# Optimization experiments

Measured on AMD Instinct MI355X. Metric: run time of the kernel, lower is better.

The kernel has to match this reference:

```python
import jax, jax.numpy as jnp
import numpy as np

ALPHA = 0.2  # LeakyReLU negative slope used throughout
NEG = -9e15


def _leaky(x, a=ALPHA):
    return jnp.where(x >= 0, x, a * x)


def _gat_layer(h, adj, W, a, concat):
    # h: [N, Fin], W: [Fin, Fout], a: [2*Fout, 1]
    Wh = h @ W                                   # [N, Fout]
    d = W.shape[-1]
    e = _leaky(Wh @ a[:d] + (Wh @ a[d:]).T)      # [N, N]
    att = jax.nn.softmax(jnp.where(adj > 0, e, NEG), axis=1)
    out = att @ Wh                               # [N, Fout]
    return jax.nn.elu(out) if concat else out


def setup_inputs() -> dict:
    key = jax.random.key(0)
    ks = jax.random.split(key, 24)
    N, F, H, D1, O1 = 4096, 512, 4, 256, 64
    x = jax.random.normal(ks[0], (N, F), dtype=jnp.float32)
    adj = jax.random.bernoulli(ks[1], 0.02, (N, N))
    adj = (adj | adj.T | jnp.eye(N, dtype=bool)).astype(jnp.float32)
    observation = jax.random.randint(ks[2], (1, N), 0, 2, dtype=jnp.int32)
    s_mat = jax.random.uniform(ks[3], (N, N), dtype=jnp.float32)
    theta = jax.random.uniform(ks[4], (1, F), dtype=jnp.float32)
    g = lambda k, s, sc: (jax.random.normal(k, s, dtype=jnp.float32) * sc)
    return {
        'x': x, 'adj': adj, 'observation': observation, 's_mat': s_mat,
        'theta': theta,
        'Wh0': g(ks[5], (H, F, D1), 0.05), 'ah0': g(ks[6], (H, 2 * D1, 1), 0.05),
        'Wh1': g(ks[7], (H, D1, D1), 0.05), 'ah1': g(ks[8], (H, 2 * D1, 1), 0.05),
        'Wo0': g(ks[9], (H * D1, O1), 0.05), 'ao0': g(ks[10], (2 * O1, 1), 0.05),
        'Wo1': g(ks[11], (O1, 1), 0.2), 'ao1': g(ks[12], (2, 1), 0.2),
        'dW': g(ks[13], (2, 10), 0.5), 'dW0': g(ks[14], (1, 10), 0.5),
        'dW1': g(ks[15], (10, 20), 0.5), 'dW01': g(ks[16], (1, 20), 0.5),
        'dW2': g(ks[17], (20, 10), 0.5), 'dW02': g(ks[18], (1, 10), 0.5),
        'dV': g(ks[19], (10, 1), 0.5), 'dV0': g(ks[20], (1, 1), 0.5),
    }


def reference(x, adj, observation, s_mat, theta, Wh0, ah0, Wh1, ah1,
              Wo0, ao0, Wo1, ao1, dW, dW0, dW1, dW01, dW2, dW02, dV, dV0):
    # mergeState: add theta to rows in the seed set (observation[0] == 1)
    seed = (observation[0] == 1).astype(x.dtype)[:, None]  # [N,1]
    h_in = x + seed * theta

    # multi-head 2-layer attention stacks (concat=True -> elu inside)
    def head(W0, a0, W1, a1):
        h = _gat_layer(h_in, adj, W0, a0, True)
        return _gat_layer(h, adj, W1, a1, True)

    hh = jax.vmap(head)(Wh0, ah0, Wh1, ah1)                 # [H, N, D1]
    hcat = jnp.transpose(hh, (1, 0, 2)).reshape(h_in.shape[0], -1)  # [N, H*D1]

    # output attention stack (concat=False), then elu (GAT.forward)
    h = _gat_layer(hcat, adj, Wo0, ao0, False)
    h = _gat_layer(h, adj, Wo1, ao1, False)
    h_ = jax.nn.elu(h)                                      # [N, 1]

    # GAT_degree v2: degreeNN over [h_, degree]
    d_v = s_mat.sum(axis=1, keepdims=True)                  # [N, 1]
    x_ = jnp.concatenate([h_, d_v], axis=1)                 # [N, 2]
    h0 = _leaky(x_ @ dW + dW0)
    h1 = _leaky(h0 @ dW1 + dW01)
    h2 = _leaky(h1 @ dW2 + dW02)
    return _leaky(h2 @ dV + dV0)                            # [N, 1]
```

## Files before the change

kernel.cpp:

```cpp
#include <hip/hip_runtime.h>
#include <hip/hip_bf16.h>
#include <hip/hip_fp16.h>
#include <math.h>

#define MAXDEG 512

typedef short v8s __attribute__((ext_vector_type(8)));
typedef float v4f __attribute__((ext_vector_type(4)));
typedef _Float16 h2 __attribute__((ext_vector_type(2)));

__device__ __forceinline__ float blockReduceSum(float v) {
    __shared__ float sh[8];
    int lane = threadIdx.x & 63, w = threadIdx.x >> 6;
    for (int o = 32; o > 0; o >>= 1) v += __shfl_down(v, o);
    __syncthreads();
    if (lane == 0) sh[w] = v;
    __syncthreads();
    if (w == 0) {
        int nw = (blockDim.x + 63) >> 6;
        v = (lane < nw) ? sh[lane] : 0.f;
        for (int o = 4; o > 0; o >>= 1) v += __shfl_down(v, o);
        if (lane == 0) sh[0] = v;
    }
    __syncthreads();
    return sh[0];
}

__device__ __forceinline__ float blockReduceMax(float v) {
    __shared__ float sh[8];
    int lane = threadIdx.x & 63, w = threadIdx.x >> 6;
    for (int o = 32; o > 0; o >>= 1) v = fmaxf(v, __shfl_down(v, o));
    __syncthreads();
    if (lane == 0) sh[w] = v;
    __syncthreads();
    if (w == 0) {
        int nw = (blockDim.x + 63) >> 6;
        v = (lane < nw) ? sh[lane] : -3.4e38f;
        for (int o = 4; o > 0; o >>= 1) v = fmaxf(v, __shfl_down(v, o));
        if (lane == 0) sh[0] = v;
    }
    __syncthreads();
    return sh[0];
}


__global__ void csr_rowsum(const float* __restrict__ adj, const float* __restrict__ s,
                           int* __restrict__ colIdx, int* __restrict__ deg,
                           float* __restrict__ dv, int N) {
    int row = blockIdx.x;
    __shared__ int cnt;
    if (threadIdx.x == 0) cnt = 0;
    __syncthreads();
    const float4* ar = (const float4*)(adj + (size_t)row * N);
    const float4* sr = (const float4*)(s + (size_t)row * N);
    int* outp = colIdx + (size_t)row * MAXDEG;
    float psum = 0.f;
    const int n4 = N >> 2;
    for (int j4 = threadIdx.x; j4 < n4; j4 += blockDim.x) {
        float4 a4 = ar[j4];
        float4 s4 = sr[j4];
        psum += (s4.x + s4.y) + (s4.z + s4.w);
        int jb = j4 << 2;
        if (a4.x > 0.f) { int p = atomicAdd(&cnt, 1); if (p < MAXDEG) outp[p] = jb; }
        if (a4.y > 0.f) { int p = atomicAdd(&cnt, 1); if (p < MAXDEG) outp[p] = jb + 1; }
        if (a4.z > 0.f) { int p = atomicAdd(&cnt, 1); if (p < MAXDEG) outp[p] = jb + 2; }
        if (a4.w > 0.f) { int p = atomicAdd(&cnt, 1); if (p < MAXDEG) outp[p] = jb + 3; }
    }
    psum = blockReduceSum(psum);
    __syncthreads();
    if (threadIdx.x == 0) {
        deg[row] = cnt < MAXDEG ? cnt : MAXDEG;
        dv[row] = psum;
    }
}

__global__ void prep(const float* __restrict__ x, const int* __restrict__ obs,
                     const float* __restrict__ theta,
                     const float* __restrict__ Wh0, const float* __restrict__ Wh1,
                     const float* __restrict__ Wo0,
                     __half* __restrict__ hin, __half* __restrict__ Wh0t,
                     __half* __restrict__ Wh1t, __half* __restrict__ Wo0t,
                     float* __restrict__ elerZ, int elerN) {
    const int n0 = 4096 * 512;
    const int n1 = 4 * 512 * 256;
    const int n2 = 4 * 256 * 256;
    const int n3 = 1024 * 64;
    int i = blockIdx.x * 256 + threadIdx.x;
    if (i < n0) {
        int n = i >> 9, f = i & 511;
        float v = x[i];
        if (obs[n] == 1) v += theta[f];
        hin[i] = __float2half(v);
    } else if (i < n0 + n1) {
        int t = i - n0;
        int b = t / (512 * 256), r = t % (512 * 256);
        int mm = r >> 9, kk = r & 511;
        Wh0t[t] = __float2half(Wh0[b * 512 * 256 + kk * 256 + mm]);
    } else if (i < n0 + n1 + n2) {
        int t = i - n0 - n1;
        int b = t >> 16, r = t & 65535;
        int mm = r >> 8, kk = r & 255;
        Wh1t[t] = __float2half(Wh1[b * 65536 + kk * 256 + mm]);
    } else if (i < n0 + n1 + n2 + n3) {
        int t = i - n0 - n1 - n2;
        int mm = t >> 10, kk = t & 1023;
        Wo0t[t] = __float2half(Wo0[kk * 64 + mm]);
    } else if (i < n0 + n1 + n2 + n3 + elerN) {
        elerZ[i - n0 - n1 - n2 - n3] = 0.f;
    }
}

__global__ __launch_bounds__(256) void gemm_mfma128(
    const __half* __restrict__ A, const __half* __restrict__ Bt,
    __half* __restrict__ C, int N, int K, int M,
    size_t sA, size_t sB, size_t sC,
    const float* __restrict__ aVec, size_t aStride,
    float* __restrict__ el, float* __restrict__ er) {
    int b = blockIdx.z;
    const unsigned short* Ag = (const unsigned short*)(A + (size_t)b * sA);
    const unsigned short* Bg = (const unsigned short*)(Bt + (size_t)b * sB);
    __half* Cg = C + (size_t)b * sC;
    const float* av = aVec + (size_t)b * aStride;

    __shared__ __align__(16) unsigned short As[128][40];
    __shared__ __align__(16) unsigned short Bs[128][40];

    const int tid = threadIdx.x;
    const int wave = tid >> 6, lane = tid & 63;
    const int wm = wave >> 1, wn = wave & 1;
    const int row0 = blockIdx.y * 128, col0 = blockIdx.x * 128;
    const int lr = tid >> 2;
    const int lo = (tid & 3) * 8;
    const int m = lane & 15, quad = lane >> 4;

    v4f acc[4][4];
    #pragma unroll
    for (int i = 0; i < 4; i++)
        #pragma unroll
        for (int c = 0; c < 4; c++) acc[i][c] = (v4f)(0.f);

    for (int k0 = 0; k0 < K; k0 += 32) {
        *(int4*)(&As[lr][lo]) =
            *(const int4*)(Ag + (size_t)(row0 + lr) * K + k0 + lo);
        *(int4*)(&As[lr + 64][lo]) =
            *(const int4*)(Ag + (size_t)(row0 + 64 + lr) * K + k0 + lo);
        *(int4*)(&Bs[lr][lo]) =
            *(const int4*)(Bg + (size_t)(col0 + lr) * K + k0 + lo);
        *(int4*)(&Bs[lr + 64][lo]) =
            *(const int4*)(Bg + (size_t)(col0 + 64 + lr) * K + k0 + lo);
        __syncthreads();
        v8s af[4], bfv[4];
        #pragma unroll
        for (int i = 0; i < 4; i++)
            af[i] = *(const v8s*)(&As[wm * 64 + i * 16 + m][quad * 8]);
        #pragma unroll
        for (int c = 0; c < 4; c++)
            bfv[c] = *(const v8s*)(&Bs[wn * 64 + c * 16 + m][quad * 8]);
        #pragma unroll
        for (int i = 0; i < 4; i++)
            #pragma unroll
            for (int c = 0; c < 4; c++)
                acc[i][c] = __builtin_amdgcn_mfma_f32_16x16x32_f16(
                    af[i], bfv[c], acc[i][c], 0, 0, 0);
        __syncthreads();
    }
    #pragma unroll
    for (int i = 0; i < 4; i++)
        #pragma unroll
        for (int c = 0; c < 4; c++)
            #pragma unroll
            for (int r = 0; r < 4; r++) {
                int row = row0 + wm * 64 + i * 16 + quad * 4 + r;
                int col = col0 + wn * 64 + c * 16 + m;
                Cg[(size_t)row * M + col] = __float2half(acc[i][c][r]);
            }
    float ael[4], aer[4];
    #pragma unroll
    for (int c = 0; c < 4; c++) {
        ael[c] = av[col0 + wn * 64 + c * 16 + m];
        aer[c] = av[M + col0 + wn * 64 + c * 16 + m];
    }
    #pragma unroll
    for (int i = 0; i < 4; i++)
        #pragma unroll
        for (int r = 0; r < 4; r++) {
            float pel = 0.f, per_ = 0.f;
            #pragma unroll
            for (int c = 0; c < 4; c++) {
                pel += acc[i][c][r] * ael[c];
                per_ += acc[i][c][r] * aer[c];
            }
            #pragma unroll
            for (int off = 1; off < 16; off <<= 1) {
                pel += __shfl_xor(pel, off);
                per_ += __shfl_xor(per_, off);
            }
            if (m == 0) {
                int row = row0 + wm * 64 + i * 16 + quad * 4 + r;
                atomicAdd(&el[(size_t)b * N + row], pel);
                atomicAdd(&er[(size_t)b * N + row], per_);
            }
        }
}

__global__ __launch_bounds__(256) void gemm_mfma64(
    const __half* __restrict__ A, const __half* __restrict__ Bt,
    __half* __restrict__ C, int N, int K, int M,
    size_t sA, size_t sB, size_t sC,
    const float* __restrict__ aVec, size_t aStride,
    float* __restrict__ el, float* __restrict__ er) {
    int b = blockIdx.z;
    const unsigned short* Ag = (const unsigned short*)(A + (size_t)b * sA);
    const unsigned short* Bg = (const unsigned short*)(Bt + (size_t)b * sB);
    __half* Cg = C + (size_t)b * sC;
    const float* av = aVec + (size_t)b * aStride;

    __shared__ __align__(16) unsigned short As[64][40];
    __shared__ __align__(16) unsigned short Bs[64][40];

    const int tid = threadIdx.x;
    const int wave = tid >> 6, lane = tid & 63;
    const int row0 = blockIdx.y * 64, col0 = blockIdx.x * 64;
    const int sRow = tid >> 2;
    const int sOff = (tid & 3) * 8;
    const int m = lane & 15, quad = lane >> 4;

    v4f acc[4];
    #pragma unroll
    for (int c = 0; c < 4; c++) acc[c] = (v4f)(0.f);

    for (int k0 = 0; k0 < K; k0 += 32) {
        *(int4*)(&As[sRow][sOff]) =
            *(const int4*)(Ag + (size_t)(row0 + sRow) * K + k0 + sOff);
        *(int4*)(&Bs[sRow][sOff]) =
            *(const int4*)(Bg + (size_t)(col0 + sRow) * K + k0 + sOff);
        __syncthreads();
        v8s af = *(const v8s*)(&As[wave * 16 + m][quad * 8]);
        #pragma unroll
        for (int c = 0; c < 4; c++) {
            v8s bfv = *(const v8s*)(&Bs[c * 16 + m][quad * 8]);
            acc[c] = __builtin_amdgcn_mfma_f32_16x16x32_f16(af, bfv, acc[c], 0, 0, 0);
        }
        __syncthreads();
    }
    #pragma unroll
    for (int c = 0; c < 4; c++)
        #pragma unroll
        for (int r = 0; r < 4; r++) {
            int row = row0 + wave * 16 + quad * 4 + r;
            int col = col0 + c * 16 + m;
            Cg[(size_t)row * M + col] = __float2half(acc[c][r]);
        }
    float ael[4], aer[4];
    #pragma unroll
    for (int c = 0; c < 4; c++) {
        ael[c] = av[col0 + c * 16 + m];
        aer[c] = av[M + col0 + c * 16 + m];
    }
    #pragma unroll
    for (int r = 0; r < 4; r++) {
        float pel = 0.f, per_ = 0.f;
        #pragma unroll
        for (int c = 0; c < 4; c++) {
            pel += acc[c][r] * ael[c];
            per_ += acc[c][r] * aer[c];
        }
        #pragma unroll
        for (int off = 1; off < 16; off <<= 1) {
            pel += __shfl_xor(pel, off);
            per_ += __shfl_xor(per_, off);
        }
        if (m == 0) {
            int row = row0 + wave * 16 + quad * 4 + r;
            atomicAdd(&el[(size_t)b * N + row], pel);
            atomicAdd(&er[(size_t)b * N + row], per_);
        }
    }
}

template<int D, int ACT, int HEADS>
__global__ __launch_bounds__(256) void attn_vec(
    const __half* __restrict__ Wh, const float* __restrict__ el,
    const float* __restrict__ er, const int* __restrict__ colIdx,
    const int* __restrict__ deg, __half* __restrict__ out,
    int N, size_t sWh, size_t sOut, int outRowStride) {
    constexpr int LPN = D / 8;
    constexpr int NPW = 64 / LPN;
    constexpr int STRIDE = 4 * NPW;
    constexpr int PAD = 2 * STRIDE;

    int b, row;
    if (HEADS == 4) {
        int blk = blockIdx.x;
        b = (blk & 7) >> 1;
        row = ((blk >> 3) << 1) | (blk & 1);
    } else {
        b = 0;
        row = blockIdx.x;
    }
    const int tid = threadIdx.x;
    const __half* whb = Wh + (size_t)b * sWh;
    const float* erb = er + (size_t)b * N;
    const float eln = el[(size_t)b * N + row];
    const int dc = deg[row];
    const int dcp = (dc + PAD - 1) & ~(PAD - 1);
    const int* ci = colIdx + (size_t)row * MAXDEG;

    __shared__ __align__(16) float2 spc[MAXDEG];
    __shared__ __align__(16) float redc[4 * D];

    float mx = -3.4e38f;
    for (int k = tid; k < dc; k += 256) {
        int j = ci[k];
        float s = eln + erb[j];
        s = fmaxf(s, 0.2f * s);
        spc[k] = make_float2(s, __int_as_float(j * (D * 2)));
        mx = fmaxf(mx, s);
    }
    for (int k = dc + tid; k < dcp; k += 256)
        spc[k] = make_float2(__int_as_float(0), __int_as_float(0));
    mx = blockReduceMax(mx);
    float l = 0.f;
    for (int k = tid; k < dc; k += 256) {
        float p = __expf(spc[k].x - mx);
        l += p;
        unsigned int pu = __half_as_ushort(__float2half(p));
        spc[k].x = __int_as_float(pu | (pu << 16));
    }
    l = blockReduceSum(l);
    const float inv = 1.f / l;

    const int wave = tid >> 6, lane = tid & 63;
    const int sub = lane / LPN;
    const int dl = (lane % LPN) * 8;
    const char* wp = (const char*)(whb + dl);

    union HU { unsigned int u; h2 h; };
    union R4 { uint4 u; h2 h[4]; };

    h2 a0[4], a1[4];
    #pragma unroll
    for (int i = 0; i < 4; i++) { a0[i] = (h2)(_Float16)0; a1[i] = (h2)(_Float16)0; }

    for (int k = wave * NPW + sub; k < dcp; k += 2 * STRIDE) {
        float2 pc0 = spc[k];
        float2 pc1 = spc[k + STRIDE];
        R4 r0, r1;
        r0.u = *(const uint4*)(wp + __float_as_int(pc0.y));
        r1.u = *(const uint4*)(wp + __float_as_int(pc1.y));
        HU p0, p1;
        p0.u = __float_as_int(pc0.x);
        p1.u = __float_as_int(pc1.x);
        #pragma unroll
        for (int i = 0; i < 4; i++) {
            a0[i] += p0.h * r0.h[i];
            a1[i] += p1.h * r1.h[i];
        }
    }
    #pragma unroll
    for (int i = 0; i < 4; i++) a0[i] += a1[i];
    #pragma unroll
    for (int off = LPN; off < 64; off <<= 1)
        #pragma unroll
        for (int i = 0; i < 4; i++) {
            HU t, s;
            t.h = a0[i];
            s.u = __shfl_xor((int)t.u, off);
            a0[i] += s.h;
        }
    __syncthreads();
    if (sub == 0)
        #pragma unroll
        for (int i = 0; i < 4; i++) {
            redc[wave * D + dl + 2 * i]     = (float)a0[i][0];
            redc[wave * D + dl + 2 * i + 1] = (float)a0[i][1];
        }
    __syncthreads();
    if (tid < D) {
        float v = (redc[tid] + redc[D + tid] + redc[2 * D + tid] + redc[3 * D + tid]) * inv;
        if (ACT == 1) v = (v > 0.f) ? v : expm1f(v);
        out[(size_t)b * sOut + (size_t)row * outRowStride + tid] = __float2half(v);
    }
}

__global__ void attn_d1(const __half* __restrict__ Wh, const float* __restrict__ el,
                        const float* __restrict__ er, const int* __restrict__ colIdx,
                        const int* __restrict__ deg, __half* __restrict__ out, int N) {
    int row = blockIdx.x, tid = threadIdx.x;
    const float eln = el[row];
    const int dc = deg[row];
    const int* ci = colIdx + (size_t)row * MAXDEG;
    __shared__ float sp[MAXDEG];
    __shared__ int sc[MAXDEG];
    float mx = -3.4e38f;
    for (int k = tid; k < dc; k += blockDim.x) {
        int j = ci[k];
        sc[k] = j;
        float s = eln + er[j];
        s = fmaxf(s, 0.2f * s);
        sp[k] = s;
        mx = fmaxf(mx, s);
    }
    mx = blockReduceMax(mx);
    float l = 0.f, acc = 0.f;
    for (int k = tid; k < dc; k += blockDim.x) {
        float p = __expf(sp[k] - mx);
        l += p;
        acc += p * __half2float(Wh[sc[k]]);
    }
    l = blockReduceSum(l);
    acc = blockReduceSum(acc);
    if (tid == 0) out[row] = __float2half(acc / l);
}

__global__ void matvec64_kernel(const __half* __restrict__ h3,
                                const float* __restrict__ w,
                                const float* __restrict__ ao1,
                                __half* __restrict__ out,
                                float* __restrict__ el4, float* __restrict__ er4, int N) {
    int row = blockIdx.x;
    float v = __half2float(h3[(size_t)row * 64 + threadIdx.x]) * w[threadIdx.x];
    for (int o = 32; o > 0; o >>= 1) v += __shfl_down(v, o);
    if (threadIdx.x == 0) {
        out[row] = __float2half(v);
        el4[row] = v * ao1[0];
        er4[row] = v * ao1[1];
    }
}

__device__ __forceinline__ float leaky(float x) { return x >= 0.f ? x : 0.2f * x; }

__global__ void degree_nn(const __half* __restrict__ h4, const float* __restrict__ dv,
                          const float* __restrict__ dW, const float* __restrict__ dW0,
                          const float* __restrict__ dW1, const float* __restrict__ dW01,
                          const float* __restrict__ dW2, const float* __restrict__ dW02,
                          const float* __restrict__ dV, const float* __restrict__ dV0,
                          float* __restrict__ out, int N) {
    int n = blockIdx.x * blockDim.x + threadIdx.x;
    if (n >= N) return;
    float h = __half2float(h4[n]);
    h = (h > 0.f) ? h : expm1f(h);
    float d = dv[n];
    float t0[10], t1[20], t2[10];
    #pragma unroll
    for (int i = 0; i < 10; i++)
        t0[i] = leaky(h * dW[i] + d * dW[10 + i] + dW0[i]);
    #pragma unroll
    for (int j = 0; j < 20; j++) {
        float s = dW01[j];
        #pragma unroll
        for (int i = 0; i < 10; i++) s += t0[i] * dW1[i * 20 + j];
        t1[j] = leaky(s);
    }
    #pragma unroll
    for (int j = 0; j < 10; j++) {
        float s = dW02[j];
        #pragma unroll
        for (int i = 0; i < 20; i++) s += t1[i] * dW2[i * 10 + j];
        t2[j] = leaky(s);
    }
    float o = dV0[0];
    #pragma unroll
    for (int i = 0; i < 10; i++) o += t2[i] * dV[i];
    out[n] = leaky(o);
}

extern "C" void kernel_launch(void* const* d_in, const int* in_sizes, int n_in,
                              void* d_out, int out_size, void* d_ws, size_t ws_size,
                              hipStream_t stream) {
    const int N = 4096, F = 512, H = 4, D1 = 256, O1 = 64;
    const float* x     = (const float*)d_in[0];
    const float* adj   = (const float*)d_in[1];
    const int*   obs   = (const int*)  d_in[2];
    const float* s_mat = (const float*)d_in[3];
    const float* theta = (const float*)d_in[4];
    const float* Wh0   = (const float*)d_in[5];
    const float* ah0   = (const float*)d_in[6];
    const float* Wh1   = (const float*)d_in[7];
    const float* ah1   = (const float*)d_in[8];
    const float* Wo0   = (const float*)d_in[9];
    const float* ao0   = (const float*)d_in[10];
    const float* Wo1   = (const float*)d_in[11];
    const float* ao1   = (const float*)d_in[12];
    const float* dWp   = (const float*)d_in[13];
    const float* dW0p  = (const float*)d_in[14];
    const float* dW1p  = (const float*)d_in[15];
    const float* dW01p = (const float*)d_in[16];
    const float* dW2p  = (const float*)d_in[17];
    const float* dW02p = (const float*)d_in[18];
    const float* dVp   = (const float*)d_in[19];
    const float* dV0p  = (const float*)d_in[20];
    float* outp = (float*)d_out;

    char* ws = (char*)d_ws;
    auto alloc = [&](size_t bytes) {
        char* p = ws;
        ws += (bytes + 255) & ~(size_t)255;
        return p;
    };
    __half* hin  = (__half*)alloc((size_t)N * F * 2);
    __half* whA  = (__half*)alloc((size_t)H * N * D1 * 2);
    __half* hb   = (__half*)alloc((size_t)H * N * D1 * 2);
    __half* hcat = (__half*)alloc((size_t)N * H * D1 * 2);
    __half* o1Wh = (__half*)alloc((size_t)N * O1 * 2);
    __half* o1o  = (__half*)alloc((size_t)N * O1 * 2);
    __half* o2Wh = (__half*)alloc((size_t)N * 2);
    __half* o2o  = (__half*)alloc((size_t)N * 2);
    __half* Wh0t = (__half*)alloc((size_t)H * F * D1 * 2);
    __half* Wh1t = (__half*)alloc((size_t)H * D1 * D1 * 2);
    __half* Wo0t = (__half*)alloc((size_t)H * D1 * O1 * 2);
    int elerN = 4 * H * N + 2 * N;
    float* elerZ = (float*)alloc((size_t)elerN * 4);
    float* el1 = elerZ;
    float* er1 = el1 + H * N;
    float* el2 = er1 + H * N;
    float* er2 = el2 + H * N;
    float* el3 = er2 + H * N;
    float* er3 = el3 + N;
    float* el4 = (float*)alloc((size_t)N * 4);
    float* er4 = (float*)alloc((size_t)N * 4);
    float* dv  = (float*)alloc((size_t)N * 4);
    int* colIdx = (int*)alloc((size_t)N * MAXDEG * 4);
    int* deg    = (int*)alloc((size_t)N * 4);

    {
        const int totalPrep = N * F + H * F * D1 + H * D1 * D1 + H * D1 * O1 + elerN;
        prep<<<(totalPrep + 255) / 256, 256, 0, stream>>>(
            x, obs, theta, Wh0, Wh1, Wo0, hin, Wh0t, Wh1t, Wo0t, elerZ, elerN);
    }
    csr_rowsum<<<N, 256, 0, stream>>>(adj, s_mat, colIdx, deg, dv, N);

    gemm_mfma128<<<dim3(D1 / 128, N / 128, H), 256, 0, stream>>>(
        hin, Wh0t, whA, N, F, D1, 0, (size_t)D1 * F, (size_t)N * D1,
        ah0, (size_t)2 * D1, el1, er1);
    attn_vec<256, 1, 4><<<N * H, 256, 0, stream>>>(
        whA, el1, er1, colIdx, deg, hb,
        N, (size_t)N * D1, (size_t)N * D1, D1);

    gemm_mfma128<<<dim3(D1 / 128, N / 128, H), 256, 0, stream>>>(
        hb, Wh1t, whA, N, D1, D1, (size_t)N * D1, (size_t)D1 * D1, (size_t)N * D1,
        ah1, (size_t)2 * D1, el2, er2);
    attn_vec<256, 1, 4><<<N * H, 256, 0, stream>>>(
        whA, el2, er2, colIdx, deg, hcat,
        N, (size_t)N * D1, (size_t)D1, H * D1);

    gemm_mfma64<<<dim3(O1 / 64, N / 64, 1), 256, 0, stream>>>(
        hcat, Wo0t, o1Wh, N, H * D1, O1, 0, 0, 0,
        ao0, 0, el3, er3);
    attn_vec<64, 0, 1><<<N, 256, 0, stream>>>(
        o1Wh, el3, er3, colIdx, deg, o1o, N, 0, 0, O1);

    matvec64_kernel<<<N, 64, 0, stream>>>(o1o, Wo1, ao1, o2Wh, el4, er4, N);
    attn_d1<<<N, 256, 0, stream>>>(o2Wh, el4, er4, colIdx, deg, o2o, N);

    degree_nn<<<(N + 255) / 256, 256, 0, stream>>>(o2o, dv, dWp, dW0p, dW1p,
        dW01p, dW2p, dW02p, dVp, dV0p, outp, N);
}
```

Baseline: 403.4 us.

## Fuse preprocessing kernels and tail kernels, widen attention gather unroll

Result: no change. 401.0 us (-0.6%).

```diff
diff --git a/kernel.cpp b/kernel.cpp
--- a/kernel.cpp
+++ b/kernel.cpp
@@ -43,49 +43,52 @@
     return sh[0];
 }
 
-
-__global__ void csr_rowsum(const float* __restrict__ adj, const float* __restrict__ s,
-                           int* __restrict__ colIdx, int* __restrict__ deg,
-                           float* __restrict__ dv, int N) {
-    int row = blockIdx.x;
-    __shared__ int cnt;
-    if (threadIdx.x == 0) cnt = 0;
-    __syncthreads();
-    const float4* ar = (const float4*)(adj + (size_t)row * N);
-    const float4* sr = (const float4*)(s + (size_t)row * N);
-    int* outp = colIdx + (size_t)row * MAXDEG;
-    float psum = 0.f;
-    const int n4 = N >> 2;
-    for (int j4 = threadIdx.x; j4 < n4; j4 += blockDim.x) {
-        float4 a4 = ar[j4];
-        float4 s4 = sr[j4];
-        psum += (s4.x + s4.y) + (s4.z + s4.w);
-        int jb = j4 << 2;
-        if (a4.x > 0.f) { int p = atomicAdd(&cnt, 1); if (p < MAXDEG) outp[p] = jb; }
-        if (a4.y > 0.f) { int p = atomicAdd(&cnt, 1); if (p < MAXDEG) outp[p] = jb + 1; }
-        if (a4.z > 0.f) { int p = atomicAdd(&cnt, 1); if (p < MAXDEG) outp[p] = jb + 2; }
-        if (a4.w > 0.f) { int p = atomicAdd(&cnt, 1); if (p < MAXDEG) outp[p] = jb + 3; }
-    }
-    psum = blockReduceSum(psum);
-    __syncthreads();
-    if (threadIdx.x == 0) {
-        deg[row] = cnt < MAXDEG ? cnt : MAXDEG;
-        dv[row] = psum;
-    }
-}
-
-__global__ void prep(const float* __restrict__ x, const int* __restrict__ obs,
-                     const float* __restrict__ theta,
-                     const float* __restrict__ Wh0, const float* __restrict__ Wh1,
-                     const float* __restrict__ Wo0,
-                     __half* __restrict__ hin, __half* __restrict__ Wh0t,
-                     __half* __restrict__ Wh1t, __half* __restrict__ Wo0t,
-                     float* __restrict__ elerZ, int elerN) {
+__device__ __forceinline__ float leaky(float x) { return x >= 0.f ? x : 0.2f * x; }
+
+
+__global__ void fused_pre(const float* __restrict__ adj, const float* __restrict__ s,
+                          int* __restrict__ colIdx, int* __restrict__ deg,
+                          float* __restrict__ dv,
+                          const float* __restrict__ x, const int* __restrict__ obs,
+                          const float* __restrict__ theta,
+                          const float* __restrict__ Wh0, const float* __restrict__ Wh1,
+                          const float* __restrict__ Wo0,
+                          __half* __restrict__ hin, __half* __restrict__ Wh0t,
+                          __half* __restrict__ Wh1t, __half* __restrict__ Wo0t,
+                          float* __restrict__ elerZ, int elerN, int N) {
+    if (blockIdx.x < 4096) {
+        int row = blockIdx.x;
+        __shared__ int cnt;
+        if (threadIdx.x == 0) cnt = 0;
+        __syncthreads();
+        const float4* ar = (const float4*)(adj + (size_t)row * N);
+        const float4* sr = (const float4*)(s + (size_t)row * N);
+        int* outp = colIdx + (size_t)row * MAXDEG;
+        float psum = 0.f;
+        const int n4 = N >> 2;
+        for (int j4 = threadIdx.x; j4 < n4; j4 += blockDim.x) {
+            float4 a4 = ar[j4];
+            float4 s4 = sr[j4];
+            psum += (s4.x + s4.y) + (s4.z + s4.w);
+            int jb = j4 << 2;
+            if (a4.x > 0.f) { int p = atomicAdd(&cnt, 1); if (p < MAXDEG) outp[p] = jb; }
+            if (a4.y > 0.f) { int p = atomicAdd(&cnt, 1); if (p < MAXDEG) outp[p] = jb + 1; }
+            if (a4.z > 0.f) { int p = atomicAdd(&cnt, 1); if (p < MAXDEG) outp[p] = jb + 2; }
+            if (a4.w > 0.f) { int p = atomicAdd(&cnt, 1); if (p < MAXDEG) outp[p] = jb + 3; }
+        }
+        psum = blockReduceSum(psum);
+        __syncthreads();
+        if (threadIdx.x == 0) {
+            deg[row] = cnt < MAXDEG ? cnt : MAXDEG;
+            dv[row] = psum;
+        }
+        return;
+    }
     const int n0 = 4096 * 512;
     const int n1 = 4 * 512 * 256;
     const int n2 = 4 * 256 * 256;
     const int n3 = 1024 * 64;
-    int i = blockIdx.x * 256 + threadIdx.x;
+    int i = (blockIdx.x - 4096) * 256 + threadIdx.x;
     if (i < n0) {
         int n = i >> 9, f = i & 511;
         float v = x[i];
@@ -278,16 +281,18 @@
     }
 }
 
-template<int D, int ACT, int HEADS>
+template<int D, int ACT, int HEADS, int FUSE>
 __global__ __launch_bounds__(256) void attn_vec(
     const __half* __restrict__ Wh, const float* __restrict__ el,
     const float* __restrict__ er, const int* __restrict__ colIdx,
     const int* __restrict__ deg, __half* __restrict__ out,
-    int N, size_t sWh, size_t sOut, int outRowStride) {
+    int N, size_t sWh, size_t sOut, int outRowStride,
+    const float* __restrict__ wo1, const float* __restrict__ ao1,
+    float* __restrict__ o2wh, float* __restrict__ el4, float* __restrict__ er4) {
     constexpr int LPN = D / 8;
-    constexpr int NPW = 64 / LPN;
-    constexpr int STRIDE = 4 * NPW;
-    constexpr int PAD = 2 * STRIDE;
+    constexpr int SUBS = 64 / LPN;
+    constexpr int PER_WAVE = SUBS * 4;
+    constexpr int PAD = 4 * PER_WAVE;
 
     int b, row;
     if (HEADS == 4) {
@@ -342,19 +347,28 @@
     #pragma unroll
     for (int i = 0; i < 4; i++) { a0[i] = (h2)(_Float16)0; a1[i] = (h2)(_Float16)0; }
 
-    for (int k = wave * NPW + sub; k < dcp; k += 2 * STRIDE) {
-        float2 pc0 = spc[k];
-        float2 pc1 = spc[k + STRIDE];
-        R4 r0, r1;
-        r0.u = *(const uint4*)(wp + __float_as_int(pc0.y));
-        r1.u = *(const uint4*)(wp + __float_as_int(pc1.y));
-        HU p0, p1;
-        p0.u = __float_as_int(pc0.x);
-        p1.u = __float_as_int(pc1.x);
+    for (int k = wave * PER_WAVE + sub * 4; k < dcp; k += PAD) {
+        float4 pA = *(const float4*)(&spc[k]);
+        float4 pB = *(const float4*)(&spc[k + 2]);
+        R4 r0, r1, r2, r3;
+        r0.u = *(const uint4*)(wp + __float_as_int(pA.y));
+        r1.u = *(const uint4*)(wp + __float_as_int(pA.w));
+        r2.u = *(const uint4*)(wp + __float_as_int(pB.y));
+        r3.u = *(const uint4*)(wp + __float_as_int(pB.w));
+        HU p0, p1, p2, p3;
+        p0.u = __float_as_int(pA.x);
+        p1.u = __float_as_int(pA.z);
+        p2.u = __float_as_int(pB.x);
+        p3.u = __float_as_int(pB.z);
         #pragma unroll
         for (int i = 0; i < 4; i++) {
             a0[i] += p0.h * r0.h[i];
-            a1[i] += p1.h * r1.h[i];
+            a1[i] += p2.h * r2.h[i];
+        }
+        #pragma unroll
+        for (int i = 0; i < 4; i++) {
+            a0[i] += p1.h * r1.h[i];
+            a1[i] += p3.h * r3.h[i];
         }
     }
     #pragma unroll
@@ -376,6 +390,20 @@
             redc[wave * D + dl + 2 * i + 1] = (float)a0[i][1];
         }
     __syncthreads();
+    if (FUSE) {
+        if (tid < 64) {
+            float vv = (redc[tid] + redc[D + tid] + redc[2 * D + tid] + redc[3 * D + tid]) * inv;
+            float t = vv * wo1[tid];
+            #pragma unroll
+            for (int o = 32; o > 0; o >>= 1) t += __shfl_down(t, o);
+            if (tid == 0) {
+                o2wh[row] = t;
+                el4[row] = t * ao1[0];
+                er4[row] = t * ao1[1];
+            }
+        }
+        return;
+    }
     if (tid < D) {
         float v = (redc[tid] + redc[D + tid] + redc[2 * D + tid] + redc[3 * D + tid]) * inv;
         if (ACT == 1) v = (v > 0.f) ? v : expm1f(v);
@@ -383,9 +411,14 @@
     }
 }
 
-__global__ void attn_d1(const __half* __restrict__ Wh, const float* __restrict__ el,
-                        const float* __restrict__ er, const int* __restrict__ colIdx,
-                        const int* __restrict__ deg, __half* __restrict__ out, int N) {
+__global__ void attn_d1_deg(const float* __restrict__ o2wh, const float* __restrict__ el,
+                            const float* __restrict__ er, const int* __restrict__ colIdx,
+                            const int* __restrict__ deg, const float* __restrict__ dv,
+                            const float* __restrict__ dW, const float* __restrict__ dW0,
+                            const float* __restrict__ dW1, const float* __restrict__ dW01,
+                            const float* __restrict__ dW2, const float* __restrict__ dW02,
+                            const float* __restrict__ dV, const float* __restrict__ dV0,
+                            float* __restrict__ out, int N) {
     int row = blockIdx.x, tid = threadIdx.x;
     const float eln = el[row];
     const int dc = deg[row];
@@ -406,63 +439,37 @@
     for (int k = tid; k < dc; k += blockDim.x) {
         float p = __expf(sp[k] - mx);
         l += p;
-        acc += p * __half2float(Wh[sc[k]]);
+        acc += p * o2wh[sc[k]];
     }
     l = blockReduceSum(l);
     acc = blockReduceSum(acc);
-    if (tid == 0) out[row] = __float2half(acc / l);
-}
-
-__global__ void matvec64_kernel(const __half* __restrict__ h3,
-                                const float* __restrict__ w,
-                                const float* __restrict__ ao1,
-                                __half* __restrict__ out,
-                                float* __restrict__ el4, float* __restrict__ er4, int N) {
-    int row = blockIdx.x;
-    float v = __half2float(h3[(size_t)row * 64 + threadIdx.x]) * w[threadIdx.x];
-    for (int o = 32; o > 0; o >>= 1) v += __shfl_down(v, o);
-    if (threadIdx.x == 0) {
-        out[row] = __float2half(v);
-        el4[row] = v * ao1[0];
-        er4[row] = v * ao1[1];
-    }
-}
-
-__device__ __forceinline__ float leaky(float x) { return x >= 0.f ? x : 0.2f * x; }
-
-__global__ void degree_nn(const __half* __restrict__ h4, const float* __restrict__ dv,
-                          const float* __restrict__ dW, const float* __restrict__ dW0,
-                          const float* __restrict__ dW1, const float* __restrict__ dW01,
-                          const float* __restrict__ dW2, const float* __restrict__ dW02,
-                          const float* __restrict__ dV, const float* __restrict__ dV0,
-                          float* __restrict__ out, int N) {
-    int n = blockIdx.x * blockDim.x + threadIdx.x;
-    if (n >= N) return;
-    float h = __half2float(h4[n]);
-    h = (h > 0.f) ? h : expm1f(h);
-    float d = dv[n];
-    float t0[10], t1[20], t2[10];
-    #pragma unroll
-    for (int i = 0; i < 10; i++)
-        t0[i] = leaky(h * dW[i] + d * dW[10 + i] + dW0[i]);
-    #pragma unroll
-    for (int j = 0; j < 20; j++) {
-        float s = dW01[j];
-        #pragma unroll
-        for (int i = 0; i < 10; i++) s += t0[i] * dW1[i * 20 + j];
-        t1[j] = leaky(s);
-    }
-    #pragma unroll
-    for (int j = 0; j < 10; j++) {
-        float s = dW02[j];
-        #pragma unroll
-        for (int i = 0; i < 20; i++) s += t1[i] * dW2[i * 10 + j];
-        t2[j] = leaky(s);
-    }
-    float o = dV0[0];
-    #pragma unroll
-    for (int i = 0; i < 10; i++) o += t2[i] * dV[i];
-    out[n] = leaky(o);
+    if (tid == 0) {
+        float h = acc / l;
+        h = (h > 0.f) ? h : expm1f(h);
+        float d = dv[row];
+        float t0[10], t1[20], t2[10];
+        #pragma unroll
+        for (int i = 0; i < 10; i++)
+            t0[i] = leaky(h * dW[i] + d * dW[10 + i] + dW0[i]);
+        #pragma unroll
+        for (int j = 0; j < 20; j++) {
+            float s = dW01[j];
+            #pragma unroll
+            for (int i = 0; i < 10; i++) s += t0[i] * dW1[i * 20 + j];
+            t1[j] = leaky(s);
+        }
+        #pragma unroll
+        for (int j = 0; j < 10; j++) {
+            float s = dW02[j];
+            #pragma unroll
+            for (int i = 0; i < 20; i++) s += t1[i] * dW2[i * 10 + j];
+            t2[j] = leaky(s);
+        }
+        float o = dV0[0];
+        #pragma unroll
+        for (int i = 0; i < 10; i++) o += t2[i] * dV[i];
+        out[row] = leaky(o);
+    }
 }
 
 extern "C" void kernel_launch(void* const* d_in, const int* in_sizes, int n_in,
@@ -503,9 +510,7 @@
     __half* hb   = (__half*)alloc((size_t)H * N * D1 * 2);
     __half* hcat = (__half*)alloc((size_t)N * H * D1 * 2);
     __half* o1Wh = (__half*)alloc((size_t)N * O1 * 2);
-    __half* o1o  = (__half*)alloc((size_t)N * O1 * 2);
-    __half* o2Wh = (__half*)alloc((size_t)N * 2);
-    __half* o2o  = (__half*)alloc((size_t)N * 2);
+    float* o2Wh  = (float*)alloc((size_t)N * 4);
     __half* Wh0t = (__half*)alloc((size_t)H * F * D1 * 2);
     __half* Wh1t = (__half*)alloc((size_t)H * D1 * D1 * 2);
     __half* Wo0t = (__half*)alloc((size_t)H * D1 * O1 * 2);
@@ -525,34 +530,36 @@
 
     {
         const int totalPrep = N * F + H * F * D1 + H * D1 * D1 + H * D1 * O1 + elerN;
-        prep<<<(totalPrep + 255) / 256, 256, 0, stream>>>(
-            x, obs, theta, Wh0, Wh1, Wo0, hin, Wh0t, Wh1t, Wo0t, elerZ, elerN);
-    }
-    csr_rowsum<<<N, 256, 0, stream>>>(adj, s_mat, colIdx, deg, dv, N);
+        const int prepBlocks = (totalPrep + 255) / 256;
+        fused_pre<<<4096 + prepBlocks, 256, 0, stream>>>(
+            adj, s_mat, colIdx, deg, dv,
+            x, obs, theta, Wh0, Wh1, Wo0, hin, Wh0t, Wh1t, Wo0t, elerZ, elerN, N);
+    }
 
     gemm_mfma128<<<dim3(D1 / 128, N / 128, H), 256, 0, stream>>>(
         hin, Wh0t, whA, N, F, D1, 0, (size_t)D1 * F, (size_t)N * D1,
         ah0, (size_t)2 * D1, el1, er1);
-    attn_vec<256, 1, 4><<<N * H, 256, 0, stream>>>(
+    attn_vec<256, 1, 4, 0><<<N * H, 256, 0, stream>>>(
         whA, el1, er1, colIdx, deg, hb,
-        N, (size_t)N * D1, (size_t)N * D1, D1);
+        N, (size_t)N * D1, (size_t)N * D1, D1,
+        nullptr, nullptr, nullptr, nullptr, nullptr);
 
     gemm_mfma128<<<dim3(D1 / 128, N / 128, H), 256, 0, stream>>>(
         hb, Wh1t, whA, N, D1, D1, (size_t)N * D1, (size_t)D1 * D1, (size_t)N * D1,
         ah1, (size_t)2 * D1, el2, er2);
-    attn_vec<256, 1, 4><<<N * H, 256, 0, stream>>>(
+    attn_vec<256, 1, 4, 0><<<N * H, 256, 0, stream>>>(
         whA, el2, er2, colIdx, deg, hcat,
-        N, (size_t)N * D1, (size_t)D1, H * D1);
+        N, (size_t)N * D1, (size_t)D1, H * D1,
+        nullptr, nullptr, nullptr, nullptr, nullptr);
 
     gemm_mfma64<<<dim3(O1 / 64, N / 64, 1), 256, 0, stream>>>(
         hcat, Wo0t, o1Wh, N, H * D1, O1, 0, 0, 0,
         ao0, 0, el3, er3);
-    attn_vec<64, 0, 1><<<N, 256, 0, stream>>>(
-        o1Wh, el3, er3, colIdx, deg, o1o, N, 0, 0, O1);
-
-    matvec64_kernel<<<N, 64, 0, stream>>>(o1o, Wo1, ao1, o2Wh, el4, er4, N);
-    attn_d1<<<N, 256, 0, stream>>>(o2Wh, el4, er4, colIdx, deg, o2o, N);
-
-    degree_nn<<<(N + 255) / 256, 256, 0, stream>>>(o2o, dv, dWp, dW0p, dW1p,
-        dW01p, dW2p, dW02p, dVp, dV0p, outp, N);
-}
+    attn_vec<64, 0, 1, 1><<<N, 256, 0, stream>>>(
+        o1Wh, el3, er3, colIdx, deg, nullptr,
+        N, 0, 0, O1,
+        Wo1, ao1, o2Wh, el4, er4);
+
+    attn_d1_deg<<<N, 256, 0, stream>>>(o2Wh, el4, er4, colIdx, deg, dv,
+        dWp, dW0p, dW1p, dW01p, dW2p, dW02p, dVp, dV0p, outp, N);
+}
```
